# Performance work log

Measured on AMD Instinct MI355X. Metric: run time of the kernel, lower is better.

## Reference

```python
import jax, jax.numpy as jnp
import numpy as np

PE_DIM = 40  # pe_dim; gaussian PE scale factor = pe_dim // 2


def _batched_linear(x, wb):
    # x: [B, N, D], wb: [B, D+1, H] (last row is bias)
    return jnp.einsum('bnd,bdh->bnh', x, wb[:, :-1, :]) + wb[:, -1:, :]


def setup_inputs() -> dict:
    key = jax.random.key(0)
    ks = jax.random.split(key, 8)
    B, N = 16, 16384
    H = 256
    pe_out = 3 * PE_DIM  # 120
    s = 0.05  # keep ReLU-chain activations bounded
    return {
        'x': jax.random.normal(ks[0], (B, N, 3), dtype=jnp.float32),
        'wb0': jax.random.normal(ks[1], (B, pe_out + 1, H), dtype=jnp.float32) * s,
        'wb1': jax.random.normal(ks[2], (B, H + 1, H), dtype=jnp.float32) * s,
        'wb2': jax.random.normal(ks[3], (B, H + 1, H), dtype=jnp.float32) * s,
        'wb3': jax.random.normal(ks[4], (B, H + 1, H), dtype=jnp.float32) * s,
        'wb4': jax.random.normal(ks[5], (B, H + 1, H), dtype=jnp.float32) * s,
        'wb_out': jax.random.normal(ks[6], (B, H + 1, 1), dtype=jnp.float32) * s,
        'rand_freqs': jax.random.normal(ks[7], (3 * (PE_DIM // 2), 3), dtype=jnp.float32),  # feat_sigma=1
    }


def reference(x, wb0, wb1, wb2, wb3, wb4, wb_out, rand_freqs):
    # Gaussian positional encoding: k = x . (rand_freqs * pe_dim//2)
    k = jnp.einsum('bnd,fd->bnf', x, rand_freqs * (PE_DIM // 2))  # [B,N,60]
    h = jnp.concatenate([jnp.sin(k), jnp.cos(k)], axis=-1)        # [B,N,120]
    for wb in (wb0, wb1, wb2, wb3, wb4):
        h = jax.nn.relu(_batched_linear(h, wb))
    out = _batched_linear(h, wb_out)  # [B,N,1]
    return out
```

## Files before the change

### kernel.cpp

```cpp
#include <hip/hip_runtime.h>
#include <hip/hip_bf16.h>


#define H 256
#define MT 128
#define PE_NF 60

typedef __attribute__((ext_vector_type(8))) short s16x8;
typedef __attribute__((ext_vector_type(4))) float f32x4;

static __device__ __forceinline__ unsigned short f2bf(float v) {
  unsigned int u = __float_as_uint(v);
  return (unsigned short)((u + 0x7FFFu + ((u >> 16) & 1u)) >> 16);
}
static __device__ __forceinline__ float bf2f(unsigned short u) {
  return __uint_as_float(((unsigned int)u) << 16);
}
static __device__ __forceinline__ int hswz(int row, int chunk) {
  return (chunk & ~7) | ((chunk ^ row) & 7);
}

__global__ __launch_bounds__(256) void prep_weights(
    const float* __restrict__ wb0, const float* __restrict__ wb1,
    const float* __restrict__ wb2, const float* __restrict__ wb3,
    const float* __restrict__ wb4,
    unsigned short* __restrict__ w0p, unsigned short* __restrict__ w14p,
    float* __restrict__ biases) {
  int z = blockIdx.z;
  int li = z >> 4, b = z & 15;
  int k0 = blockIdx.x * 32;
  int n0 = blockIdx.y * 32;
  int Ks;
  const float* src;
  unsigned short* dst;
  if (li == 0) {
    Ks = 120;
    if (k0 >= 128) return;
    src = wb0 + (size_t)b * 121 * H;
    dst = w0p + (size_t)b * 32768;
  } else {
    Ks = 256;
    const float* srcs[4] = {wb1, wb2, wb3, wb4};
    src = srcs[li - 1] + (size_t)b * 257 * H;
    dst = w14p + ((size_t)(li - 1) * 16 + b) * 65536;
  }
  __shared__ float tile[32][33];
  int t = threadIdx.x;
  int tx = t & 31, ty = t >> 5;
#pragma unroll
  for (int i = 0; i < 4; ++i) {
    int k = k0 + ty + i * 8;
    tile[ty + i * 8][tx] = (k < Ks) ? src[(size_t)k * H + n0 + tx] : 0.f;
  }
  if (k0 == 0 && ty == 0)
    biases[((size_t)li * 16 + b) * H + n0 + tx] = src[(size_t)Ks * H + n0 + tx];
  __syncthreads();
  if (t < 128) {
    int nn = t & 31, kg = t >> 5;
    int n = n0 + nn;
    int kt = k0 >> 5;
    int w = n >> 6, ct = (n >> 4) & 3, rl = n & 15;
    union { unsigned short us[8]; s16x8 v; } pk;
#pragma unroll
    for (int j = 0; j < 8; ++j) pk.us[j] = f2bf(tile[kg * 8 + j][nn]);
    *(s16x8*)&dst[(size_t)(kt * 16 + w * 4 + ct) * 512 + (kg * 16 + rl) * 8] = pk.v;
  }
}

template <int NKT, bool LAST>
static __device__ __forceinline__ void mlp_layer(
    const unsigned short* __restrict__ wl, const unsigned short* __restrict__ wln,
    const float* __restrict__ bl, unsigned short* __restrict__ h_s,
    const int rlane, const int kgrp, const int w, const int l,
    s16x8 (&bb)[2][4]) {
  static_assert((NKT & 1) == 0, "ping-pong parity needs even NKT");
  const int n_base = w * 64;

  f32x4 acc[8][4];
  {
    f32x4 bini[4];
#pragma unroll
    for (int ct = 0; ct < 4; ++ct)
      bini[ct] = *(const f32x4*)(bl + n_base + ct * 16 + kgrp * 4);
#pragma unroll
    for (int rt = 0; rt < 8; ++rt)
#pragma unroll
      for (int ct = 0; ct < 4; ++ct) acc[rt][ct] = bini[ct];
  }

  const unsigned short* fp = wl + (size_t)(w * 4) * 512 + l * 8;
  int aoff[8];
#pragma unroll
  for (int rt = 0; rt < 8; ++rt) aoff[rt] = (rt * 16 + rlane) * 256;

#pragma unroll
  for (int kt = 0; kt < NKT; ++kt) {
    if (kt + 1 < NKT) {
#pragma unroll
      for (int ct = 0; ct < 4; ++ct)
        bb[(kt + 1) & 1][ct] = *(const s16x8*)(fp + (kt + 1) * 8192 + ct * 512);
    } else if (!LAST) {
      const unsigned short* fpn = wln + (size_t)(w * 4) * 512 + l * 8;
#pragma unroll
      for (int ct = 0; ct < 4; ++ct)
        bb[0][ct] = *(const s16x8*)(fpn + ct * 512);
    }
    s16x8 afr[8];
    const int cs = hswz(rlane, kt * 4 + kgrp) * 8;
#pragma unroll
    for (int rt = 0; rt < 8; ++rt)
      afr[rt] = *(const s16x8*)&h_s[aoff[rt] + cs];
    __builtin_amdgcn_s_setprio(1);
#pragma unroll
    for (int rt = 0; rt < 8; ++rt)
#pragma unroll
      for (int ct = 0; ct < 4; ++ct)
        acc[rt][ct] = __builtin_amdgcn_mfma_f32_16x16x32_bf16(
            bb[kt & 1][ct], afr[rt], acc[rt][ct], 0, 0, 0);
    __builtin_amdgcn_s_setprio(0);
  }
  __syncthreads();

  const int sub = (kgrp & 1) * 4;
  const int cbase = w * 8 + (kgrp >> 1);
#pragma unroll
  for (int rt = 0; rt < 8; ++rt) {
    const int m = rt * 16 + rlane;
    const int rowb = m * 256;
#pragma unroll
    for (int ct = 0; ct < 4; ++ct) {
      const int cs = hswz(m, cbase + ct * 2);
      float v0 = fmaxf(acc[rt][ct][0], 0.f);
      float v1 = fmaxf(acc[rt][ct][1], 0.f);
      float v2 = fmaxf(acc[rt][ct][2], 0.f);
      float v3 = fmaxf(acc[rt][ct][3], 0.f);
      union { __hip_bfloat162 h2[2]; uint2 u; } pk;
      pk.h2[0] = __float22bfloat162_rn(float2{v0, v1});
      pk.h2[1] = __float22bfloat162_rn(float2{v2, v3});
      *(uint2*)&h_s[rowb + cs * 8 + sub] = pk.u;
    }
  }
  __syncthreads();
}

__global__ __launch_bounds__(256, 2) void hyponerf_main(
    const float* __restrict__ x, const float* __restrict__ rfreq,
    const float* __restrict__ wbout,
    const unsigned short* __restrict__ w0p, const unsigned short* __restrict__ w14p,
    const float* __restrict__ biases, float* __restrict__ out) {
  __shared__ __align__(16) unsigned short h_s[MT * 256];
  __shared__ float fr_s[PE_NF * 3];
  __shared__ float x_s[MT * 3];
  __shared__ float wout_s[H + 1];

  int bid = blockIdx.x;
  int logical = (bid & 7) * 256 + (bid >> 3);
  int b  = logical >> 7;
  int mt = logical & 127;

  int t = threadIdx.x;
  int w = t >> 6, l = t & 63;
  int rlane = l & 15;
  int kgrp  = l >> 4;

  const unsigned short* wl0 = w0p + (size_t)b * 32768;
  const unsigned short* wl1 = w14p + (size_t)(0 * 16 + b) * 65536;
  const unsigned short* wl2 = w14p + (size_t)(1 * 16 + b) * 65536;
  const unsigned short* wl3 = w14p + (size_t)(2 * 16 + b) * 65536;
  const unsigned short* wl4 = w14p + (size_t)(3 * 16 + b) * 65536;

  s16x8 bb[2][4];
  {
    const unsigned short* fp0 = wl0 + (size_t)(w * 4) * 512 + l * 8;
#pragma unroll
    for (int ct = 0; ct < 4; ++ct) bb[0][ct] = *(const s16x8*)(fp0 + ct * 512);
  }

  const float* xg = x + ((size_t)b * 16384 + (size_t)mt * MT) * 3;
  for (int i = t; i < MT * 3; i += 256) x_s[i] = xg[i];
  for (int i = t; i < PE_NF * 3; i += 256) fr_s[i] = rfreq[i] * 20.0f;
  for (int i = t; i < H + 1; i += 256) wout_s[i] = wbout[(size_t)b * (H + 1) + i];
  __syncthreads();

  {
    int r = t >> 1;
    int q = t & 1;
    float x0 = x_s[r * 3 + 0], x1 = x_s[r * 3 + 1], x2 = x_s[r * 3 + 2];
    int rowb = r * 256;
#pragma unroll
    for (int cc = 0; cc < 8; ++cc) {
      union { unsigned short us[8]; s16x8 v; } pk;
#pragma unroll
      for (int j = 0; j < 8; ++j) {
        int n = q * 64 + cc * 8 + j;
        float v = 0.f;
        if (n < 60) {
          float kv = x0 * fr_s[n * 3] + x1 * fr_s[n * 3 + 1] + x2 * fr_s[n * 3 + 2];
          v = __sinf(kv);
        } else if (n < 120) {
          int f = n - 60;
          float kv = x0 * fr_s[f * 3] + x1 * fr_s[f * 3 + 1] + x2 * fr_s[f * 3 + 2];
          v = __cosf(kv);
        }
        pk.us[j] = f2bf(v);
      }
      *(s16x8*)&h_s[rowb + hswz(r, q * 8 + cc) * 8] = pk.v;
    }
  }
  __syncthreads();

  mlp_layer<4, false>(wl0, wl1, biases + (size_t)(0 * 16 + b) * H, h_s,
                      rlane, kgrp, w, l, bb);
  mlp_layer<8, false>(wl1, wl2, biases + (size_t)(1 * 16 + b) * H, h_s,
                      rlane, kgrp, w, l, bb);
  mlp_layer<8, false>(wl2, wl3, biases + (size_t)(2 * 16 + b) * H, h_s,
                      rlane, kgrp, w, l, bb);
  mlp_layer<8, false>(wl3, wl4, biases + (size_t)(3 * 16 + b) * H, h_s,
                      rlane, kgrp, w, l, bb);
  mlp_layer<8, true >(wl4, wl4, biases + (size_t)(4 * 16 + b) * H, h_s,
                      rlane, kgrp, w, l, bb);

  {
    int r = t >> 1;
    int cb = (t & 1) * 16;
    int rowb = r * 256;
    float sum = 0.f;
#pragma unroll
    for (int c = 0; c < 16; ++c) {
      int ch = cb + c;
      const s16x8 hv = *(const s16x8*)&h_s[rowb + hswz(r, ch) * 8];
#pragma unroll
      for (int j = 0; j < 8; ++j)
        sum += bf2f((unsigned short)hv[j]) * wout_s[ch * 8 + j];
    }
    sum += __shfl_xor(sum, 1);
    if ((t & 1) == 0)
      out[(size_t)b * 16384 + (size_t)mt * MT + r] = sum + wout_s[H];
  }
}

extern "C" void kernel_launch(void* const* d_in, const int* in_sizes, int n_in,
                              void* d_out, int out_size, void* d_ws, size_t ws_size,
                              hipStream_t stream) {
  const float* x     = (const float*)d_in[0];
  const float* wb0   = (const float*)d_in[1];
  const float* wb1   = (const float*)d_in[2];
  const float* wb2   = (const float*)d_in[3];
  const float* wb3   = (const float*)d_in[4];
  const float* wb4   = (const float*)d_in[5];
  const float* wbout = (const float*)d_in[6];
  const float* rfreq = (const float*)d_in[7];
  float* out = (float*)d_out;

  char* ws = (char*)d_ws;
  unsigned short* w0p  = (unsigned short*)ws;
  unsigned short* w14p = (unsigned short*)(ws + (size_t)16 * 32768 * 2);
  float* biases = (float*)(ws + (size_t)16 * 32768 * 2
                              + (size_t)64 * 65536 * 2);

  prep_weights<<<dim3(8, 8, 80), 256, 0, stream>>>(wb0, wb1, wb2, wb3, wb4,
                                                   w0p, w14p, biases);
  hyponerf_main<<<dim3(2048), 256, 0, stream>>>(x, rfreq, wbout, w0p, w14p,
                                                biases, out);
}
```

Measured before the change: 173.3 us.

## Give each wave a private 32-row slab covering all 256 columns, removing block barriers

The work split changes from waves sharing a 128-row tile, each wave computing 64 output columns, to each wave owning 32 rows and computing all 256 columns in a private LDS slab. Because each wave only reads and writes its own rows, the two __syncthreads per layer and the one after the positional encoding are dropped. The weight prepack layout changes to match, and weight fragments are streamed in half-tile groups of 8 from global/L2. In exchange, each wave now loads the full weight matrix instead of a quarter, so weight traffic rises fourfold, and 32 accumulators per lane plus 16 weight fragments add register pressure.

```diff
diff --git a/kernel.cpp b/kernel.cpp
--- a/kernel.cpp
+++ b/kernel.cpp
@@ -3,7 +3,6 @@
 
 
 #define H 256
-#define MT 128
 #define PE_NF 60
 
 typedef __attribute__((ext_vector_type(8))) short s16x8;
@@ -59,77 +58,82 @@
     int nn = t & 31, kg = t >> 5;
     int n = n0 + nn;
     int kt = k0 >> 5;
-    int w = n >> 6, ct = (n >> 4) & 3, rl = n & 15;
+    int ct = n >> 4, rl = n & 15;
     union { unsigned short us[8]; s16x8 v; } pk;
 #pragma unroll
     for (int j = 0; j < 8; ++j) pk.us[j] = f2bf(tile[kg * 8 + j][nn]);
-    *(s16x8*)&dst[(size_t)(kt * 16 + w * 4 + ct) * 512 + (kg * 16 + rl) * 8] = pk.v;
+    *(s16x8*)&dst[(size_t)(kt * 16 + ct) * 512 + (kg * 16 + rl) * 8] = pk.v;
   }
 }
 
 template <int NKT, bool LAST>
 static __device__ __forceinline__ void mlp_layer(
-    const unsigned short* __restrict__ wl, const unsigned short* __restrict__ wln,
-    const float* __restrict__ bl, unsigned short* __restrict__ h_s,
-    const int rlane, const int kgrp, const int w, const int l,
-    s16x8 (&bb)[2][4]) {
-  static_assert((NKT & 1) == 0, "ping-pong parity needs even NKT");
-  const int n_base = w * 64;
-
-  f32x4 acc[8][4];
-  {
-    f32x4 bini[4];
-#pragma unroll
-    for (int ct = 0; ct < 4; ++ct)
-      bini[ct] = *(const f32x4*)(bl + n_base + ct * 16 + kgrp * 4);
-#pragma unroll
-    for (int rt = 0; rt < 8; ++rt)
-#pragma unroll
-      for (int ct = 0; ct < 4; ++ct) acc[rt][ct] = bini[ct];
-  }
-
-  const unsigned short* fp = wl + (size_t)(w * 4) * 512 + l * 8;
-  int aoff[8];
-#pragma unroll
-  for (int rt = 0; rt < 8; ++rt) aoff[rt] = (rt * 16 + rlane) * 256;
+    const unsigned short* __restrict__ wl,
+    const unsigned short* __restrict__ wln,
+    const float* __restrict__ bl,
+    unsigned short* __restrict__ slab,
+    const int rlane, const int kgrp, const int l,
+    s16x8 (&wf)[2][8]) {
+  f32x4 acc[2][16];
+#pragma unroll
+  for (int ct = 0; ct < 16; ++ct) {
+    f32x4 bini = *(const f32x4*)(bl + ct * 16 + kgrp * 4);
+    acc[0][ct] = bini;
+    acc[1][ct] = bini;
+  }
+  const unsigned short* fp = wl + l * 8;
+
+  s16x8 af[2][2];
+  {
+    const int cs = hswz(rlane, kgrp) * 8;
+    af[0][0] = *(const s16x8*)&slab[rlane * 256 + cs];
+    af[0][1] = *(const s16x8*)&slab[(16 + rlane) * 256 + cs];
+  }
 
 #pragma unroll
   for (int kt = 0; kt < NKT; ++kt) {
-    if (kt + 1 < NKT) {
-#pragma unroll
-      for (int ct = 0; ct < 4; ++ct)
-        bb[(kt + 1) & 1][ct] = *(const s16x8*)(fp + (kt + 1) * 8192 + ct * 512);
-    } else if (!LAST) {
-      const unsigned short* fpn = wln + (size_t)(w * 4) * 512 + l * 8;
-#pragma unroll
-      for (int ct = 0; ct < 4; ++ct)
-        bb[0][ct] = *(const s16x8*)(fpn + ct * 512);
-    }
-    s16x8 afr[8];
-    const int cs = hswz(rlane, kt * 4 + kgrp) * 8;
-#pragma unroll
-    for (int rt = 0; rt < 8; ++rt)
-      afr[rt] = *(const s16x8*)&h_s[aoff[rt] + cs];
-    __builtin_amdgcn_s_setprio(1);
-#pragma unroll
-    for (int rt = 0; rt < 8; ++rt)
-#pragma unroll
-      for (int ct = 0; ct < 4; ++ct)
-        acc[rt][ct] = __builtin_amdgcn_mfma_f32_16x16x32_bf16(
-            bb[kt & 1][ct], afr[rt], acc[rt][ct], 0, 0, 0);
-    __builtin_amdgcn_s_setprio(0);
-  }
-  __syncthreads();
-
-  const int sub = (kgrp & 1) * 4;
-  const int cbase = w * 8 + (kgrp >> 1);
-#pragma unroll
-  for (int rt = 0; rt < 8; ++rt) {
+#pragma unroll
+    for (int half = 0; half < 2; ++half) {
+      if (half == 0) {
+#pragma unroll
+        for (int c = 0; c < 8; ++c)
+          wf[1][c] = *(const s16x8*)(fp + (kt * 16 + 8 + c) * 512);
+        if (kt + 1 < NKT) {
+          const int cs = hswz(rlane, (kt + 1) * 4 + kgrp) * 8;
+          af[(kt + 1) & 1][0] = *(const s16x8*)&slab[rlane * 256 + cs];
+          af[(kt + 1) & 1][1] = *(const s16x8*)&slab[(16 + rlane) * 256 + cs];
+        }
+      } else {
+        if (kt + 1 < NKT) {
+#pragma unroll
+          for (int c = 0; c < 8; ++c)
+            wf[0][c] = *(const s16x8*)(fp + ((kt + 1) * 16 + c) * 512);
+        } else if (!LAST) {
+          const unsigned short* fpn = wln + l * 8;
+#pragma unroll
+          for (int c = 0; c < 8; ++c)
+            wf[0][c] = *(const s16x8*)(fpn + c * 512);
+        }
+      }
+      __builtin_amdgcn_s_setprio(1);
+#pragma unroll
+      for (int c = 0; c < 8; ++c) {
+        acc[0][half * 8 + c] = __builtin_amdgcn_mfma_f32_16x16x32_bf16(
+            wf[half][c], af[kt & 1][0], acc[0][half * 8 + c], 0, 0, 0);
+        acc[1][half * 8 + c] = __builtin_amdgcn_mfma_f32_16x16x32_bf16(
+            wf[half][c], af[kt & 1][1], acc[1][half * 8 + c], 0, 0, 0);
+      }
+      __builtin_amdgcn_s_setprio(0);
+    }
+  }
+
+#pragma unroll
+  for (int rt = 0; rt < 2; ++rt) {
     const int m = rt * 16 + rlane;
     const int rowb = m * 256;
 #pragma unroll
-    for (int ct = 0; ct < 4; ++ct) {
-      const int cs = hswz(m, cbase + ct * 2);
+    for (int ct = 0; ct < 16; ++ct) {
+      const int cs = hswz(m, ct * 2 + (kgrp >> 1));
       float v0 = fmaxf(acc[rt][ct][0], 0.f);
       float v1 = fmaxf(acc[rt][ct][1], 0.f);
       float v2 = fmaxf(acc[rt][ct][2], 0.f);
@@ -137,10 +141,9 @@
       union { __hip_bfloat162 h2[2]; uint2 u; } pk;
       pk.h2[0] = __float22bfloat162_rn(float2{v0, v1});
       pk.h2[1] = __float22bfloat162_rn(float2{v2, v3});
-      *(uint2*)&h_s[rowb + cs * 8 + sub] = pk.u;
-    }
-  }
-  __syncthreads();
+      *(uint2*)&slab[rowb + cs * 8 + (kgrp & 1) * 4] = pk.u;
+    }
+  }
 }
 
 __global__ __launch_bounds__(256, 2) void hyponerf_main(
@@ -148,9 +151,8 @@
     const float* __restrict__ wbout,
     const unsigned short* __restrict__ w0p, const unsigned short* __restrict__ w14p,
     const float* __restrict__ biases, float* __restrict__ out) {
-  __shared__ __align__(16) unsigned short h_s[MT * 256];
+  __shared__ __align__(16) unsigned short h_s[4 * 32 * 256];
   __shared__ float fr_s[PE_NF * 3];
-  __shared__ float x_s[MT * 3];
   __shared__ float wout_s[H + 1];
 
   int bid = blockIdx.x;
@@ -162,6 +164,7 @@
   int w = t >> 6, l = t & 63;
   int rlane = l & 15;
   int kgrp  = l >> 4;
+  unsigned short* slab = h_s + w * 32 * 256;
 
   const unsigned short* wl0 = w0p + (size_t)b * 32768;
   const unsigned short* wl1 = w14p + (size_t)(0 * 16 + b) * 65536;
@@ -169,30 +172,31 @@
   const unsigned short* wl3 = w14p + (size_t)(2 * 16 + b) * 65536;
   const unsigned short* wl4 = w14p + (size_t)(3 * 16 + b) * 65536;
 
-  s16x8 bb[2][4];
-  {
-    const unsigned short* fp0 = wl0 + (size_t)(w * 4) * 512 + l * 8;
-#pragma unroll
-    for (int ct = 0; ct < 4; ++ct) bb[0][ct] = *(const s16x8*)(fp0 + ct * 512);
-  }
-
-  const float* xg = x + ((size_t)b * 16384 + (size_t)mt * MT) * 3;
-  for (int i = t; i < MT * 3; i += 256) x_s[i] = xg[i];
+  s16x8 wf[2][8];
+  {
+    const unsigned short* fp0 = wl0 + l * 8;
+#pragma unroll
+    for (int c = 0; c < 8; ++c) wf[0][c] = *(const s16x8*)(fp0 + c * 512);
+  }
+
   for (int i = t; i < PE_NF * 3; i += 256) fr_s[i] = rfreq[i] * 20.0f;
   for (int i = t; i < H + 1; i += 256) wout_s[i] = wbout[(size_t)b * (H + 1) + i];
   __syncthreads();
 
   {
-    int r = t >> 1;
-    int q = t & 1;
-    float x0 = x_s[r * 3 + 0], x1 = x_s[r * 3 + 1], x2 = x_s[r * 3 + 2];
+    int r = l >> 1;
+    int q = l & 1;
+    int grow = mt * 128 + w * 32 + r;
+    const float* xr = x + ((size_t)b * 16384 + grow) * 3;
+    float x0 = xr[0], x1 = xr[1], x2 = xr[2];
     int rowb = r * 256;
 #pragma unroll
     for (int cc = 0; cc < 8; ++cc) {
+      int ch = q * 8 + cc;
       union { unsigned short us[8]; s16x8 v; } pk;
 #pragma unroll
       for (int j = 0; j < 8; ++j) {
-        int n = q * 64 + cc * 8 + j;
+        int n = ch * 8 + j;
         float v = 0.f;
         if (n < 60) {
           float kv = x0 * fr_s[n * 3] + x1 * fr_s[n * 3 + 1] + x2 * fr_s[n * 3 + 2];
@@ -204,38 +208,37 @@
         }
         pk.us[j] = f2bf(v);
       }
-      *(s16x8*)&h_s[rowb + hswz(r, q * 8 + cc) * 8] = pk.v;
-    }
-  }
-  __syncthreads();
-
-  mlp_layer<4, false>(wl0, wl1, biases + (size_t)(0 * 16 + b) * H, h_s,
-                      rlane, kgrp, w, l, bb);
-  mlp_layer<8, false>(wl1, wl2, biases + (size_t)(1 * 16 + b) * H, h_s,
-                      rlane, kgrp, w, l, bb);
-  mlp_layer<8, false>(wl2, wl3, biases + (size_t)(2 * 16 + b) * H, h_s,
-                      rlane, kgrp, w, l, bb);
-  mlp_layer<8, false>(wl3, wl4, biases + (size_t)(3 * 16 + b) * H, h_s,
-                      rlane, kgrp, w, l, bb);
-  mlp_layer<8, true >(wl4, wl4, biases + (size_t)(4 * 16 + b) * H, h_s,
-                      rlane, kgrp, w, l, bb);
-
-  {
-    int r = t >> 1;
-    int cb = (t & 1) * 16;
+      *(s16x8*)&slab[rowb + hswz(r, ch) * 8] = pk.v;
+    }
+  }
+
+  mlp_layer<4, false>(wl0, wl1, biases + (size_t)(0 * 16 + b) * H, slab,
+                      rlane, kgrp, l, wf);
+  mlp_layer<8, false>(wl1, wl2, biases + (size_t)(1 * 16 + b) * H, slab,
+                      rlane, kgrp, l, wf);
+  mlp_layer<8, false>(wl2, wl3, biases + (size_t)(2 * 16 + b) * H, slab,
+                      rlane, kgrp, l, wf);
+  mlp_layer<8, false>(wl3, wl4, biases + (size_t)(3 * 16 + b) * H, slab,
+                      rlane, kgrp, l, wf);
+  mlp_layer<8, true >(wl4, wl4, biases + (size_t)(4 * 16 + b) * H, slab,
+                      rlane, kgrp, l, wf);
+
+  {
+    int r = l >> 1;
+    int q = l & 1;
     int rowb = r * 256;
     float sum = 0.f;
 #pragma unroll
     for (int c = 0; c < 16; ++c) {
-      int ch = cb + c;
-      const s16x8 hv = *(const s16x8*)&h_s[rowb + hswz(r, ch) * 8];
+      int ch = q * 16 + c;
+      const s16x8 hv = *(const s16x8*)&slab[rowb + hswz(r, ch) * 8];
 #pragma unroll
       for (int j = 0; j < 8; ++j)
         sum += bf2f((unsigned short)hv[j]) * wout_s[ch * 8 + j];
     }
     sum += __shfl_xor(sum, 1);
-    if ((t & 1) == 0)
-      out[(size_t)b * 16384 + (size_t)mt * MT + r] = sum + wout_s[H];
+    if (q == 0)
+      out[(size_t)b * 16384 + mt * 128 + w * 32 + r] = sum + wout_s[H];
   }
 }
 
```

Result: slower. 211.3 us (+21.9%).
